# Optimization experiments

Hardware: AMD Instinct MI355X
Metric: run time of the kernel (lower is better)

## Reference

```python
import jax, jax.numpy as jnp
import numpy as np

B, T, P, H = 32, 4096, 512, 512  # batch, frames, phonemes, hidden


def setup_inputs() -> dict:
    key = jax.random.key(0)
    ks = jax.random.split(key, 10)
    encoder_out = jax.random.normal(ks[0], (B, P, H), dtype=jnp.float32)
    pitch = jax.random.normal(ks[1], (B, T), dtype=jnp.float32)
    beats = jax.random.normal(ks[2], (B, T), dtype=jnp.float32)
    align_phone = jnp.sort(jax.random.randint(ks[3], (B, T), 0, P, dtype=jnp.int32), axis=1)
    s = 1.0  # Linear(1,H) fan_in=1 init scale
    w_pitch = jax.random.uniform(ks[4], (H,), jnp.float32, -s, s)
    b_pitch = jax.random.uniform(ks[5], (H,), jnp.float32, -s, s)
    w_beats = jax.random.uniform(ks[6], (H,), jnp.float32, -s, s)
    b_beats = jax.random.uniform(ks[7], (H,), jnp.float32, -s, s)
    w_pos = jax.random.uniform(ks[8], (H,), jnp.float32, -s, s)
    b_pos = jax.random.uniform(ks[9], (H,), jnp.float32, -s, s)
    return {
        "encoder_out": encoder_out, "pitch": pitch, "beats": beats,
        "w_pitch": w_pitch, "b_pitch": b_pitch,
        "w_beats": w_beats, "b_beats": b_beats,
        "w_pos": w_pos, "b_pos": b_pos,
        "align_phone": align_phone,
    }


def _align(encoder_out, align_phone):
    # length-regulator: encoder index = running count of change points in align_phone
    Bn, Tn = align_phone.shape
    change = jnp.concatenate(
        [jnp.zeros((Bn, 1), jnp.int32),
         (align_phone[:, 1:] != align_phone[:, :-1]).astype(jnp.int32)], axis=1)
    idx = jnp.clip(jnp.cumsum(change, axis=1), 0, encoder_out.shape[1] - 1)  # [B,T]
    return jnp.take_along_axis(encoder_out, idx[:, :, None], axis=1)  # [B,T,H]


def reference(encoder_out, pitch, beats, w_pitch, b_pitch, w_beats, b_beats,
              w_pos, b_pos, align_phone):
    aligned = _align(encoder_out, align_phone)              # [B,T,H]
    out = aligned
    out = out + (pitch[..., None] * w_pitch + b_pitch)      # fc_pitch
    out = out + (beats[..., None] * w_beats + b_beats)      # fc_beats
    pos = jnp.arange(aligned.shape[1], dtype=aligned.dtype)[:, None]  # [T,1]
    out = out + (pos * w_pos + b_pos)                       # fc_pos on positions
    return out
```

## Files before the change

kernel.cpp:

```cpp
#include <hip/hip_runtime.h>

constexpr int B = 32;
constexpr int T = 4096;
constexpr int P = 512;
constexpr int H = 512;
constexpr int H4 = H / 4;
constexpr int LOG2_H4 = 7;
constexpr int LOG2_T = 12;

__global__ __launch_bounds__(256) void scan_idx_kernel(
    const int* __restrict__ align, int* __restrict__ idx) {
  const int b = blockIdx.x;
  const int tid = threadIdx.x;
  const long base = (long)b * T;
  constexpr int CH = T / 256;
  const int start = tid * CH;

  int local[CH];
  int prev = align[base + (start > 0 ? start - 1 : 0)];
  int run = 0;
#pragma unroll
  for (int j = 0; j < CH; ++j) {
    int a = align[base + start + j];
    run += ((start + j) > 0 && a != prev) ? 1 : 0;
    prev = a;
    local[j] = run;
  }

  __shared__ int sums[256];
  sums[tid] = run;
  __syncthreads();
  for (int off = 1; off < 256; off <<= 1) {
    int v = (tid >= off) ? sums[tid - off] : 0;
    __syncthreads();
    sums[tid] += v;
    __syncthreads();
  }
  const int excl = (tid > 0) ? sums[tid - 1] : 0;

#pragma unroll
  for (int j = 0; j < CH; ++j) {
    int v = excl + local[j];
    idx[base + start + j] = (v > (P - 1)) ? (P - 1) : v;
  }
}

__global__ __launch_bounds__(256) void fuse_kernel(
    const float4* __restrict__ enc,
    const float* __restrict__ pitch,
    const float* __restrict__ beats,
    const float4* __restrict__ wp, const float4* __restrict__ bp,
    const float4* __restrict__ wb, const float4* __restrict__ bb,
    const float4* __restrict__ wpos, const float4* __restrict__ bpos,
    const int* __restrict__ idx,
    float4* __restrict__ out) {
  const long total4 = (long)B * T * H4;
  long i = (long)blockIdx.x * blockDim.x + threadIdx.x;
  const long stride = (long)gridDim.x * blockDim.x;

  for (; i < total4; i += stride) {
    const int col = (int)(i & (H4 - 1));
    const long row = i >> LOG2_H4;
    const int t = (int)(row & (T - 1));
    const int b = (int)(row >> LOG2_T);

    const int e = idx[row];
    const float p = pitch[row];
    const float q = beats[row];
    const float tf = (float)t;

    const float4 ev = enc[((long)(b * P + e) << LOG2_H4) + col];
    const float4 w1 = wp[col], c1 = bp[col];
    const float4 w2 = wb[col], c2 = bb[col];
    const float4 w3 = wpos[col], c3 = bpos[col];

    float4 o;
    o.x = ev.x + fmaf(p, w1.x, c1.x) + fmaf(q, w2.x, c2.x) + fmaf(tf, w3.x, c3.x);
    o.y = ev.y + fmaf(p, w1.y, c1.y) + fmaf(q, w2.y, c2.y) + fmaf(tf, w3.y, c3.y);
    o.z = ev.z + fmaf(p, w1.z, c1.z) + fmaf(q, w2.z, c2.z) + fmaf(tf, w3.z, c3.z);
    o.w = ev.w + fmaf(p, w1.w, c1.w) + fmaf(q, w2.w, c2.w) + fmaf(tf, w3.w, c3.w);
    out[i] = o;
  }
}

extern "C" void kernel_launch(void* const* d_in, const int* in_sizes, int n_in,
                              void* d_out, int out_size, void* d_ws, size_t ws_size,
                              hipStream_t stream) {
  const float* enc     = (const float*)d_in[0];
  const float* pitch   = (const float*)d_in[1];
  const float* beats   = (const float*)d_in[2];
  const float* w_pitch = (const float*)d_in[3];
  const float* b_pitch = (const float*)d_in[4];
  const float* w_beats = (const float*)d_in[5];
  const float* b_beats = (const float*)d_in[6];
  const float* w_pos   = (const float*)d_in[7];
  const float* b_pos   = (const float*)d_in[8];
  const int* align     = (const int*)d_in[9];

  int* idx = (int*)d_ws;

  scan_idx_kernel<<<B, 256, 0, stream>>>(align, idx);

  const long total4 = (long)B * T * H4;
  const int block = 256;
  const int grid = 2048;
  fuse_kernel<<<grid, block, 0, stream>>>(
      (const float4*)enc, pitch, beats,
      (const float4*)w_pitch, (const float4*)b_pitch,
      (const float4*)w_beats, (const float4*)b_beats,
      (const float4*)w_pos, (const float4*)b_pos,
      idx, (float4*)d_out);
  (void)in_sizes; (void)n_in; (void)out_size; (void)ws_size; (void)total4;
}
```

Measured before the change: 374.3 us.

## Pack per-row index, pitch, beats, position into float4 and remap rows per XCD

The scan kernel now writes one float4 per row holding the precomputed encoder row offset, pitch, beats and the position value. The fuse kernel reads that single record with a wave-uniform (readfirstlane) index. It hoists the weights and a pre-summed bias out of the loop and assigns contiguous row ranges to each of the 8 XCDs, with two rows per block iteration. This is meant to cut scattered per-element scalar loads and index arithmetic and to improve L2 locality of encoder rows. The cost is a larger workspace and more work in the small serial scan kernel.

```diff
diff --git a/kernel.cpp b/kernel.cpp
--- a/kernel.cpp
+++ b/kernel.cpp
@@ -6,10 +6,12 @@
 constexpr int H = 512;
 constexpr int H4 = H / 4;
 constexpr int LOG2_H4 = 7;
-constexpr int LOG2_T = 12;
 
 __global__ __launch_bounds__(256) void scan_idx_kernel(
-    const int* __restrict__ align, int* __restrict__ idx) {
+    const int* __restrict__ align,
+    const float* __restrict__ pitch,
+    const float* __restrict__ beats,
+    float4* __restrict__ packed) {
   const int b = blockIdx.x;
   const int tid = threadIdx.x;
   const long base = (long)b * T;
@@ -41,45 +43,57 @@
 #pragma unroll
   for (int j = 0; j < CH; ++j) {
     int v = excl + local[j];
-    idx[base + start + j] = (v > (P - 1)) ? (P - 1) : v;
+    v = (v > (P - 1)) ? (P - 1) : v;
+    float4 pk;
+    pk.x = __int_as_float((b * P + v) << LOG2_H4);
+    pk.y = pitch[base + start + j];
+    pk.z = beats[base + start + j];
+    pk.w = (float)(start + j);
+    packed[base + start + j] = pk;
   }
 }
 
 __global__ __launch_bounds__(256) void fuse_kernel(
     const float4* __restrict__ enc,
-    const float* __restrict__ pitch,
-    const float* __restrict__ beats,
+    const float4* __restrict__ packed,
     const float4* __restrict__ wp, const float4* __restrict__ bp,
     const float4* __restrict__ wb, const float4* __restrict__ bb,
     const float4* __restrict__ wpos, const float4* __restrict__ bpos,
-    const int* __restrict__ idx,
     float4* __restrict__ out) {
-  const long total4 = (long)B * T * H4;
-  long i = (long)blockIdx.x * blockDim.x + threadIdx.x;
-  const long stride = (long)gridDim.x * blockDim.x;
+  const int tid = threadIdx.x;
+  const int col = tid & (H4 - 1);
+  const int rowHalf = tid >> 7;
 
-  for (; i < total4; i += stride) {
-    const int col = (int)(i & (H4 - 1));
-    const long row = i >> LOG2_H4;
-    const int t = (int)(row & (T - 1));
-    const int b = (int)(row >> LOG2_T);
+  const float4 w1 = wp[col], w2 = wb[col], w3 = wpos[col];
+  float4 cs;
+  {
+    const float4 c1 = bp[col], c2 = bb[col], c3 = bpos[col];
+    cs.x = c1.x + c2.x + c3.x;
+    cs.y = c1.y + c2.y + c3.y;
+    cs.z = c1.z + c2.z + c3.z;
+    cs.w = c1.w + c2.w + c3.w;
+  }
 
-    const int e = idx[row];
-    const float p = pitch[row];
-    const float q = beats[row];
-    const float tf = (float)t;
+  const int bid = blockIdx.x;
+  const int xcd = bid & 7;
+  const int lb = bid >> 3;
+  constexpr int ROWS_PER_XCD = (B * T) / 8;
+  int r = xcd * ROWS_PER_XCD + lb * 2 + rowHalf;
+  const int rEnd = xcd * ROWS_PER_XCD + ROWS_PER_XCD;
 
-    const float4 ev = enc[((long)(b * P + e) << LOG2_H4) + col];
-    const float4 w1 = wp[col], c1 = bp[col];
-    const float4 w2 = wb[col], c2 = bb[col];
-    const float4 w3 = wpos[col], c3 = bpos[col];
+  for (; r < rEnd; r += 512) {
+    const int rU = __builtin_amdgcn_readfirstlane(r);
+    const float4 pk = packed[rU];
+    const int ebase = __float_as_int(pk.x);
+    const float4 ev = enc[ebase + col];
 
     float4 o;
-    o.x = ev.x + fmaf(p, w1.x, c1.x) + fmaf(q, w2.x, c2.x) + fmaf(tf, w3.x, c3.x);
-    o.y = ev.y + fmaf(p, w1.y, c1.y) + fmaf(q, w2.y, c2.y) + fmaf(tf, w3.y, c3.y);
-    o.z = ev.z + fmaf(p, w1.z, c1.z) + fmaf(q, w2.z, c2.z) + fmaf(tf, w3.z, c3.z);
-    o.w = ev.w + fmaf(p, w1.w, c1.w) + fmaf(q, w2.w, c2.w) + fmaf(tf, w3.w, c3.w);
-    out[i] = o;
+    o.x = ev.x + fmaf(pk.y, w1.x, fmaf(pk.z, w2.x, fmaf(pk.w, w3.x, cs.x)));
+    o.y = ev.y + fmaf(pk.y, w1.y, fmaf(pk.z, w2.y, fmaf(pk.w, w3.y, cs.y)));
+    o.z = ev.z + fmaf(pk.y, w1.z, fmaf(pk.z, w2.z, fmaf(pk.w, w3.z, cs.z)));
+    o.w = ev.w + fmaf(pk.y, w1.w, fmaf(pk.z, w2.w, fmaf(pk.w, w3.w, cs.w)));
+
+    out[((long)r << LOG2_H4) + col] = o;
   }
 }
 
@@ -97,18 +111,15 @@
   const float* b_pos   = (const float*)d_in[8];
   const int* align     = (const int*)d_in[9];
 
-  int* idx = (int*)d_ws;
+  float4* packed = (float4*)d_ws;
 
-  scan_idx_kernel<<<B, 256, 0, stream>>>(align, idx);
+  scan_idx_kernel<<<B, 256, 0, stream>>>(align, pitch, beats, packed);
 
-  const long total4 = (long)B * T * H4;
-  const int block = 256;
-  const int grid = 2048;
-  fuse_kernel<<<grid, block, 0, stream>>>(
-      (const float4*)enc, pitch, beats,
+  fuse_kernel<<<2048, 256, 0, stream>>>(
+      (const float4*)enc, packed,
       (const float4*)w_pitch, (const float4*)b_pitch,
       (const float4*)w_beats, (const float4*)b_beats,
       (const float4*)w_pos, (const float4*)b_pos,
-      idx, (float4*)d_out);
-  (void)in_sizes; (void)n_in; (void)out_size; (void)ws_size; (void)total4;
+      (float4*)d_out);
+  (void)in_sizes; (void)n_in; (void)out_size; (void)ws_size;
 }
```

Result: faster. 329.3 us (-12.0%).
